# Kernel tuning notes

Hardware: AMD Instinct MI355X
Metric: run time of the kernel (lower is better)

The kernel has to match this reference:

```python
import jax, jax.numpy as jnp
import numpy as np

EMBED = 1024
ADIM = 1024
H = 16
HD = ADIM // H          # 64
RAY = 48                # ray_subdim
R = RAY // 3            # 16
SCALE = 1.0 / np.sqrt(HD)
NB = 768                # boundary tokens
MN = 8                  # max neighbors
FG = 6                  # face_group
L = 1024                # tokens per face
B = 12                  # b * face_group
STAGES = 4


def _apply_dray(x, d, einsum_str, inverse):
    ray = x[..., :RAY].reshape(x.shape[:-1] + (3, R))
    if inverse:
        d = jnp.swapaxes(d, -1, -2)
    ray = jnp.einsum(einsum_str, d, ray).reshape(x.shape[:-1] + (RAY,))
    return jnp.concatenate([ray, x[..., RAY:]], axis=-1)


def setup_inputs() -> dict:
    key = jax.random.key(0)
    ks = jax.random.split(key, 12)
    inp = {}
    inp['x'] = jax.random.normal(ks[0], (B, L, EMBED), dtype=jnp.float32)
    inp['qkv_w'] = jax.random.normal(ks[1], (EMBED, 3 * ADIM), dtype=jnp.float32) * 0.02
    inp['out_w'] = jax.random.normal(ks[2], (ADIM, EMBED), dtype=jnp.float32) * 0.02
    inp['out_b'] = jax.random.normal(ks[3], (EMBED,), dtype=jnp.float32) * 0.02
    inp['d_ray'] = jax.random.normal(ks[4], (STAGES, FG, L, 3, 3), dtype=jnp.float32)
    inp['boundary_face_ids'] = jax.random.randint(ks[5], (NB,), 0, FG, dtype=jnp.int32).astype(jnp.int64)
    inp['boundary_token_indices'] = jnp.arange(NB, dtype=jnp.int64)
    inp['boundary_local_indices'] = jax.random.randint(ks[6], (NB,), 0, L, dtype=jnp.int32).astype(jnp.int64)
    inp['boundary_stage_ids'] = jax.random.randint(ks[7], (NB,), 0, STAGES, dtype=jnp.int32).astype(jnp.int64)
    inp['neighbor_face_ids'] = jax.random.randint(ks[8], (NB, MN), 0, FG, dtype=jnp.int32).astype(jnp.int64)
    inp['neighbor_token_indices'] = jax.random.randint(ks[9], (NB, MN), 0, L, dtype=jnp.int32).astype(jnp.int64)
    inp['neighbor_local_indices'] = jax.random.randint(ks[10], (NB, MN), 0, L, dtype=jnp.int32).astype(jnp.int64)
    inp['neighbor_stage_ids'] = jax.random.randint(ks[11], (NB, MN), 0, STAGES, dtype=jnp.int32).astype(jnp.int64)
    inp['neighbor_mask'] = jnp.ones((NB, MN), dtype=bool)
    inp['face_group'] = FG
    return inp


def reference(x, qkv_w, out_w, out_b, d_ray,
              boundary_face_ids, boundary_token_indices, boundary_local_indices, boundary_stage_ids,
              neighbor_face_ids, neighbor_token_indices, neighbor_local_indices, neighbor_stage_ids,
              neighbor_mask, face_group):
    b = x.shape[0] // face_group
    l = x.shape[1]
    xt = x.reshape(b, face_group, l, EMBED)          # [b, FG, L, E]
    max_face, max_idx = face_group - 1, l - 1

    qf = jnp.clip(boundary_face_ids, 0, max_face)
    qi = jnp.clip(boundary_token_indices, 0, max_idx)
    valid_q = (boundary_face_ids == qf) & (boundary_token_indices == qi)

    nf = jnp.clip(neighbor_face_ids, 0, max_face)
    ni = jnp.clip(neighbor_token_indices, 0, max_idx)
    mask = neighbor_mask & (neighbor_face_ids == nf) & (neighbor_token_indices == ni)

    # gather boundary queries and neighbor keys/values
    x_q = xt[:, qf, qi, :]                            # [b, NB, E]
    x_kv = xt[:, nf, ni, :]                           # [b, NB, MN, E]
    q = (x_q @ qkv_w)[..., :ADIM]
    kv = x_kv @ qkv_w
    k = kv[..., ADIM:2 * ADIM]
    v = kv[..., 2 * ADIM:]

    nb, mn = q.shape[1], k.shape[2]
    q = q.reshape(b, nb, H, HD)
    k = k.reshape(b, nb, mn, H, HD)
    v = v.reshape(b, nb, mn, H, HD)

    d_q = d_ray[boundary_stage_ids, boundary_face_ids, boundary_local_indices]     # [NB, 3, 3]
    d_k = d_ray[neighbor_stage_ids,
                jnp.maximum(neighbor_face_ids, 0),
                jnp.maximum(neighbor_local_indices, 0)]                            # [NB, MN, 3, 3]

    q = _apply_dray(q, d_q, 'nij,bnhjr->bnhir', inverse=False)
    k = _apply_dray(k, d_k, 'nmij,bnmhjr->bnmhir', inverse=False)
    v = _apply_dray(v, d_k, 'nmij,bnmhjr->bnmhir', inverse=False)

    attn = jnp.einsum('bnhd,bnmhd->bnmh', q, k) * SCALE
    attn = jnp.where(mask[None, :, :, None], attn, -jnp.inf)
    attn = jax.nn.softmax(attn, axis=2)               # softmax over neighbors
    out = jnp.einsum('bnmh,bnmhd->bnhd', attn, v)

    out = _apply_dray(out, d_q, 'nij,bnhjr->bnhir', inverse=True)
    out = out.reshape(b, nb, ADIM) @ out_w + out_b
    out = out * valid_q[None, :, None].astype(out.dtype)

    out_full = jnp.zeros_like(xt).at[:, qf, qi, :].set(out)
    return out_full.reshape(-1, l, EMBED)
```

## Files before the change

### kernel.cpp

```cpp
#include <hip/hip_runtime.h>
#include <hip/hip_bf16.h>
#include <cstddef>

#define FG 6
#define L 1024
#define NB 768
#define MN 8
#define H 16
#define HD 64
#define ADIM 1024
#define STAGES 4
#define SCALE 0.125f

typedef __attribute__((ext_vector_type(8))) short bf16x8;
typedef __attribute__((ext_vector_type(4))) float f32x4;
typedef __attribute__((address_space(3))) short lds_short_t;
typedef const __attribute__((address_space(1))) short g_short_t;

__device__ __forceinline__ int clampi(int v, int lo, int hi) {
  return v < lo ? lo : (v > hi ? hi : v);
}

__device__ __forceinline__ short f2bf(float f) {
  __hip_bfloat16 h = __float2bfloat16(f);
  return *reinterpret_cast<short*>(&h);
}

__device__ __forceinline__ float bf2f(short s) {
  __hip_bfloat16 h = *reinterpret_cast<__hip_bfloat16*>(&s);
  return __bfloat162float(h);
}

__device__ __forceinline__ void gload16(const short* g, short* l) {
  __builtin_amdgcn_global_load_lds((g_short_t*)g, (lds_short_t*)l, 16, 0, 0);
}

__global__ __launch_bounds__(256)
void prep_kernel(const float* __restrict__ in, short* __restrict__ out,
                 float* __restrict__ zout) {
  const size_t zi = ((size_t)blockIdx.x * 256 + threadIdx.x) * 4;
  *(float4*)(zout + zi) = (float4){0.f, 0.f, 0.f, 0.f};
  if (blockIdx.x >= 6144) return;
  size_t i = ((size_t)blockIdx.x * 256 + threadIdx.x) * 8;
  float4 a = *(const float4*)(in + i);
  float4 b = *(const float4*)(in + i + 4);
  bf16x8 v;
  v[0] = f2bf(a.x); v[1] = f2bf(a.y); v[2] = f2bf(a.z); v[3] = f2bf(a.w);
  v[4] = f2bf(b.x); v[5] = f2bf(b.y); v[6] = f2bf(b.z); v[7] = f2bf(b.w);
  *(bf16x8*)(out + i) = v;
}

__global__ __launch_bounds__(256)
void transpose_both(const float* __restrict__ qkv_w, short* __restrict__ qwT,
                    const float* __restrict__ out_w, short* __restrict__ owT) {
  const int z = blockIdx.z;
  if (z == 1 && blockIdx.x >= 32) return;
  const float* in = z ? out_w : qkv_w;
  short* out = z ? owT : qwT;
  const int N = z ? 1024 : 3072;
  __shared__ float tile[32][33];
  const int n0 = blockIdx.x * 32, k0 = blockIdx.y * 32;
  const int tx = threadIdx.x & 31, ty = threadIdx.x >> 5;
  #pragma unroll
  for (int i = 0; i < 4; ++i)
    tile[ty + i * 8][tx] = in[(size_t)(k0 + ty + i * 8) * N + n0 + tx];
  __syncthreads();
  #pragma unroll
  for (int i = 0; i < 4; ++i)
    out[(size_t)(n0 + ty + i * 8) * 1024 + k0 + tx] =
        f2bf(tile[tx][ty + i * 8]);
}

__global__ __launch_bounds__(256)
void q_gemm64(const short* __restrict__ A, const short* __restrict__ B,
              float* __restrict__ C,
              const int* __restrict__ f_ids, const int* __restrict__ t_ids)
{
  __shared__ __align__(16) short As[4096];
  __shared__ __align__(16) short Bs[8192];

  const int tid = threadIdx.x;
  const int w = tid >> 6, lane = tid & 63;
  const int row0 = blockIdx.y * 64, col0 = blockIdx.x * 128;
  const int lr = lane & 15, lq = lane >> 4;
  const int wrow = (w >> 1) * 32, wcol = (w & 1) * 64;

  size_t asrc[2]; short* adst[2];
  #pragma unroll
  for (int c = 0; c < 2; ++c) {
    const int d = c * 256 + tid, r = d >> 3;
    const int ss = (d & 7) ^ (r & 7);
    const int rr = row0 + r;
    const int bi = rr >= NB;
    const int idx = rr - bi * NB;
    const int f = clampi(f_ids[idx], 0, FG - 1);
    const int q = clampi(t_ids[idx], 0, L - 1);
    asrc[c] = (size_t)((bi * FG + f) * L + q) * 1024 + ss * 8;
    adst[c] = As + d * 8;
  }
  size_t bsrc[4]; short* bdst[4];
  #pragma unroll
  for (int c = 0; c < 4; ++c) {
    const int d = c * 256 + tid, r = d >> 3;
    const int ss = (d & 7) ^ (r & 7);
    bsrc[c] = (size_t)(col0 + r) * 1024 + ss * 8;
    bdst[c] = Bs + d * 8;
  }

  const char* As8 = (const char*)As;
  const char* Bs8 = (const char*)Bs;
  const int swz = lr & 7;

  f32x4 acc[2][4];
  #pragma unroll
  for (int m = 0; m < 2; ++m)
    #pragma unroll
    for (int n = 0; n < 4; ++n) acc[m][n] = (f32x4){0.f, 0.f, 0.f, 0.f};

  for (int kt = 0; kt < 16; ++kt) {
    #pragma unroll
    for (int c = 0; c < 2; ++c) gload16(A + asrc[c] + kt * 64, adst[c]);
    #pragma unroll
    for (int c = 0; c < 4; ++c) gload16(B + bsrc[c] + kt * 64, bdst[c]);
    __syncthreads();
    #pragma unroll
    for (int kk = 0; kk < 2; ++kk) {
      const int so = ((kk * 4 + lq) ^ swz) << 4;
      bf16x8 av[2], bv[4];
      #pragma unroll
      for (int m = 0; m < 2; ++m)
        av[m] = *(const bf16x8*)(As8 + (wrow + m * 16 + lr) * 128 + so);
      #pragma unroll
      for (int n = 0; n < 4; ++n)
        bv[n] = *(const bf16x8*)(Bs8 + (wcol + n * 16 + lr) * 128 + so);
      #pragma unroll
      for (int m = 0; m < 2; ++m)
        #pragma unroll
        for (int n = 0; n < 4; ++n)
          acc[m][n] = __builtin_amdgcn_mfma_f32_16x16x32_bf16(
              av[m], bv[n], acc[m][n], 0, 0, 0);
    }
    __syncthreads();
  }

  #pragma unroll
  for (int m = 0; m < 2; ++m)
    #pragma unroll
    for (int j = 0; j < 4; ++j) {
      const int r = row0 + wrow + m * 16 + lq * 4 + j;
      #pragma unroll
      for (int n = 0; n < 4; ++n)
        C[(size_t)r * 1024 + col0 + wcol + n * 16 + lr] = acc[m][n][j];
    }
}

#define BAR()   do { __builtin_amdgcn_s_barrier(); __builtin_amdgcn_sched_barrier(0); } while (0)
#define LGKM(N) do { asm volatile("s_waitcnt lgkmcnt(" #N ")" ::: "memory"); __builtin_amdgcn_sched_barrier(0); } while (0)
#define VMC(N)  do { asm volatile("s_waitcnt vmcnt(" #N ")" ::: "memory"); __builtin_amdgcn_sched_barrier(0); } while (0)
#define PRIO1   __builtin_amdgcn_s_setprio(1)
#define PRIO0   __builtin_amdgcn_s_setprio(0)

#define LDA6(D, FB, KK, BUF)                                                  \
  { _Pragma("unroll")                                                         \
    for (int f_ = 0; f_ < 3; ++f_) {                                          \
      const int row_ = (2 * ((FB) + f_) + wm) * 16 + lr;                      \
      D[f_] = *(const bf16x8*)(As8 + (BUF) * 24576 + row_ * 128               \
               + ((((KK) * 4 + lq) ^ swz) << 4));                             \
    } }

#define LDB4(D, KK, BUF)                                                      \
  { _Pragma("unroll")                                                         \
    for (int g_ = 0; g_ < 4; ++g_) {                                          \
      const int row_ = wn * 64 + g_ * 16 + lr;                                \
      D[g_] = *(const bf16x8*)(Bs8 + (BUF) * 32768 + row_ * 128               \
               + ((((KK) * 4 + lq) ^ swz) << 4));                             \
    } }

#define MM6(AV, BV, FB)                                                       \
  { _Pragma("unroll")                                                         \
    for (int f_ = 0; f_ < 3; ++f_)                                            \
      _Pragma("unroll")                                                       \
      for (int g_ = 0; g_ < 4; ++g_)                                          \
        acc[(FB) + f_][g_] = __builtin_amdgcn_mfma_f32_16x16x32_bf16(         \
            AV[f_], BV[g_], acc[(FB) + f_][g_], 0, 0, 0); }

__global__ __launch_bounds__(512, 2)
void kv_gemm192(const short* __restrict__ A, const short* __restrict__ B,
                short* __restrict__ C,
                const int* __restrict__ f_ids, const int* __restrict__ t_ids)
{
  __shared__ __align__(16) short As[24576];
  __shared__ __align__(16) short Bs[32768];

  const int tid = threadIdx.x;
  const int w = tid >> 6, lane = tid & 63;
  const int wm = w >> 2, wn = w & 3;
  const int lr = lane & 15, lq = lane >> 4;
  const int row0 = blockIdx.y * 192;
  const int col0 = blockIdx.x * 256;

  const int ssrc = (((tid & 7) ^ ((tid >> 3) & 7))) * 8;

  size_t a_src[3];
  #pragma unroll
  for (int c = 0; c < 3; ++c) {
    const int rr = row0 + c * 64 + (tid >> 3);
    const int bi = rr >= NB * MN;
    const int idx = rr - bi * (NB * MN);
    const int f = clampi(f_ids[idx], 0, FG - 1);
    const int q = clampi(t_ids[idx], 0, L - 1);
    a_src[c] = (size_t)((bi * FG + f) * L + q) * 1024 + ssrc;
  }
  size_t b_src[2][2];
  #pragma unroll
  for (int h = 0; h < 2; ++h)
    #pragma unroll
    for (int i = 0; i < 2; ++i)
      b_src[h][i] = (size_t)(1024 + col0 + h * 128 + ((tid + i * 512) >> 3)) * 1024 + ssrc;

  auto stgA = [&](int c, int kt, int buf) {
    gload16(A + a_src[c] + kt * 64, As + buf * 12288 + c * 4096 + tid * 8);
  };
  auto stgB = [&](int h, int kt, int buf) {
    gload16(B + b_src[h][0] + kt * 64, Bs + buf * 16384 + h * 8192 + tid * 8);
    gload16(B + b_src[h][1] + kt * 64, Bs + buf * 16384 + h * 8192 + 4096 + tid * 8);
  };

  const char* As8 = (const char*)As;
  const char* Bs8 = (const char*)Bs;
  const int swz = lane & 7;

  f32x4 acc[6][4];
  #pragma unroll
  for (int f = 0; f < 6; ++f)
    #pragma unroll
    for (int g = 0; g < 4; ++g) acc[f][g] = (f32x4){0.f, 0.f, 0.f, 0.f};

  bf16x8 avA[3], avB[3], bv0[4], bv1[4];

  stgB(0, 0, 0); stgB(1, 0, 0); stgA(0, 0, 0); stgA(1, 0, 0); stgA(2, 0, 0);
  stgB(0, 1, 1); stgB(1, 1, 1); stgA(0, 1, 1);
  VMC(5); BAR();

  for (int I = 0; I < 7; ++I) {
    const int kA = 2 * I + 1, kB = 2 * I + 2, kC = 2 * I + 3;
    LDA6(avA, 0, 0, 0); LDB4(bv0, 0, 0); stgA(1, kA, 1);
    BAR(); LGKM(0); PRIO1; MM6(avA, bv0, 0); PRIO0; BAR();
    LDA6(avB, 0, 1, 0); LDB4(bv1, 1, 0); stgA(2, kA, 1);
    BAR(); LGKM(0); PRIO1; MM6(avB, bv1, 0); PRIO0; BAR();
    LDA6(avA, 3, 0, 0); stgB(0, kB, 0);
    BAR(); LGKM(0); PRIO1; MM6(avA, bv0, 3); PRIO0; BAR();
    LDA6(avB, 3, 1, 0); stgB(1, kB, 0); stgA(0, kB, 0);
    BAR(); LGKM(0); PRIO1; MM6(avB, bv1, 3); PRIO0; VMC(5); BAR();
    LDA6(avA, 0, 0, 1); LDB4(bv0, 0, 1); stgA(1, kB, 0);
    BAR(); LGKM(0); PRIO1; MM6(avA, bv0, 0); PRIO0; BAR();
    LDA6(avB, 0, 1, 1); LDB4(bv1, 1, 1); stgA(2, kB, 0);
    BAR(); LGKM(0); PRIO1; MM6(avB, bv1, 0); PRIO0; BAR();
    LDA6(avA, 3, 0, 1); stgB(0, kC, 1);
    BAR(); LGKM(0); PRIO1; MM6(avA, bv0, 3); PRIO0; BAR();
    LDA6(avB, 3, 1, 1); stgB(1, kC, 1); stgA(0, kC, 1);
    BAR(); LGKM(0); PRIO1; MM6(avB, bv1, 3); PRIO0; VMC(5); BAR();
  }

  {
    LDA6(avA, 0, 0, 0); LDB4(bv0, 0, 0); stgA(1, 15, 1);
    BAR(); LGKM(0); PRIO1; MM6(avA, bv0, 0); PRIO0; BAR();

    LDA6(avB, 0, 1, 0); LDB4(bv1, 1, 0); stgA(2, 15, 1);
    BAR(); LGKM(0); PRIO1; MM6(avB, bv1, 0); PRIO0; BAR();

    LDA6(avA, 3, 0, 0);
    BAR(); LGKM(0); PRIO1; MM6(avA, bv0, 3); PRIO0; BAR();

    LDA6(avB, 3, 1, 0);
    BAR(); LGKM(0); PRIO1; MM6(avB, bv1, 3); PRIO0; VMC(0); BAR();

    LDA6(avA, 0, 0, 1); LDB4(bv0, 0, 1);
    BAR(); LGKM(0); PRIO1; MM6(avA, bv0, 0); PRIO0; BAR();

    LDA6(avB, 0, 1, 1); LDB4(bv1, 1, 1);
    BAR(); LGKM(0); PRIO1; MM6(avB, bv1, 0); PRIO0; BAR();

    LDA6(avA, 3, 0, 1);
    BAR(); LGKM(0); PRIO1; MM6(avA, bv0, 3); PRIO0; BAR();

    LDA6(avB, 3, 1, 1);
    BAR(); LGKM(0); PRIO1; MM6(avB, bv1, 3); PRIO0;
  }

  #pragma unroll
  for (int f = 0; f < 6; ++f) {
    #pragma unroll
    for (int j = 0; j < 4; ++j) {
      const int r = row0 + (2 * f + wm) * 16 + lq * 4 + j;
      short* cp = C + (size_t)r * 2048 + col0 + wn * 64 + lr;
      #pragma unroll
      for (int g = 0; g < 4; ++g)
        cp[g * 16] = f2bf(acc[f][g][j]);
    }
  }
}

__global__ __launch_bounds__(256)
void out_gemm64(const short* __restrict__ A, const short* __restrict__ B,
                float* __restrict__ C,
                const int* __restrict__ f_ids, const int* __restrict__ t_ids,
                const float* __restrict__ bias)
{
  __shared__ __align__(16) short As[4096];
  __shared__ __align__(16) short Bs[8192];

  const int tid = threadIdx.x;
  const int w = tid >> 6, lane = tid & 63;
  const int row0 = blockIdx.y * 64, col0 = blockIdx.x * 128;
  const int lr = lane & 15, lq = lane >> 4;
  const int wrow = (w >> 1) * 32, wcol = (w & 1) * 64;

  size_t asrc[2]; short* adst[2];
  #pragma unroll
  for (int c = 0; c < 2; ++c) {
    const int d = c * 256 + tid, r = d >> 3;
    const int ss = (d & 7) ^ (r & 7);
    asrc[c] = (size_t)(row0 + r) * 1024 + ss * 8;
    adst[c] = As + d * 8;
  }
  size_t bsrc[4]; short* bdst[4];
  #pragma unroll
  for (int c = 0; c < 4; ++c) {
    const int d = c * 256 + tid, r = d >> 3;
    const int ss = (d & 7) ^ (r & 7);
    bsrc[c] = (size_t)(col0 + r) * 1024 + ss * 8;
    bdst[c] = Bs + d * 8;
  }

  const char* As8 = (const char*)As;
  const char* Bs8 = (const char*)Bs;
  const int swz = lr & 7;

  f32x4 acc[2][4];
  #pragma unroll
  for (int m = 0; m < 2; ++m)
    #pragma unroll
    for (int n = 0; n < 4; ++n) acc[m][n] = (f32x4){0.f, 0.f, 0.f, 0.f};

  for (int kt = 0; kt < 16; ++kt) {
    #pragma unroll
    for (int c = 0; c < 2; ++c) gload16(A + asrc[c] + kt * 64, adst[c]);
    #pragma unroll
    for (int c = 0; c < 4; ++c) gload16(B + bsrc[c] + kt * 64, bdst[c]);
    __syncthreads();
    #pragma unroll
    for (int kk = 0; kk < 2; ++kk) {
      const int so = ((kk * 4 + lq) ^ swz) << 4;
      bf16x8 av[2], bv[4];
      #pragma unroll
      for (int m = 0; m < 2; ++m)
        av[m] = *(const bf16x8*)(As8 + (wrow + m * 16 + lr) * 128 + so);
      #pragma unroll
      for (int n = 0; n < 4; ++n)
        bv[n] = *(const bf16x8*)(Bs8 + (wcol + n * 16 + lr) * 128 + so);
      #pragma unroll
      for (int m = 0; m < 2; ++m)
        #pragma unroll
        for (int n = 0; n < 4; ++n)
          acc[m][n] = __builtin_amdgcn_mfma_f32_16x16x32_bf16(
              av[m], bv[n], acc[m][n], 0, 0, 0);
    }
    __syncthreads();
  }

  float bb[4];
  #pragma unroll
  for (int n = 0; n < 4; ++n) bb[n] = bias[col0 + wcol + n * 16 + lr];
  #pragma unroll
  for (int m = 0; m < 2; ++m)
    #pragma unroll
    for (int j = 0; j < 4; ++j) {
      const int r  = row0 + wrow + m * 16 + lq * 4 + j;
      const int bi = r >= NB;
      const int nn = r - bi * NB;
      const int bf = f_ids[nn], bt = t_ids[nn];
      const int qf = clampi(bf, 0, FG - 1), qi = clampi(bt, 0, L - 1);
      const bool valid = (bf == qf) && (bt == qi);
      const size_t obase = ((size_t)(bi * FG + qf) * L + qi) * 1024;
      #pragma unroll
      for (int n = 0; n < 4; ++n) {
        const int col = col0 + wcol + n * 16 + lr;
        C[obase + col] = valid ? (acc[m][n][j] + bb[n]) : 0.f;
      }
    }
}

__global__ __launch_bounds__(256)
void attn_kernel2(const float* __restrict__ dray,
                  const int* __restrict__ bfid, const int* __restrict__ blid,
                  const int* __restrict__ bsid,
                  const int* __restrict__ nfid, const int* __restrict__ ntid,
                  const int* __restrict__ nlid, const int* __restrict__ nsid,
                  const int* __restrict__ nmask,
                  const float* __restrict__ qbuf,
                  const short* __restrict__ kvbuf,
                  __hip_bfloat16* __restrict__ obuf)
{
  __shared__ __align__(16) short kvlds[MN * 2048];
  __shared__ float smdq[9];
  __shared__ float smdk[MN][9];
  __shared__ int   smok[MN];

  const int bn   = blockIdx.x;
  const int n    = bn % NB;
  const int tid  = threadIdx.x;
  const int w    = tid >> 6, lane = tid & 63;

  const short* kvb = kvbuf + (size_t)bn * MN * 2048;
  #pragma unroll
  for (int j = 0; j < 8; ++j)
    gload16(kvb + (j * 256 + tid) * 8, kvlds + (j * 256 + tid) * 8);

  if (tid < 9) {
    int st = clampi(bsid[n], 0, STAGES - 1);
    int f  = clampi(bfid[n], 0, FG - 1);
    int lc = clampi(blid[n], 0, L - 1);
    smdq[tid] = dray[((size_t)(st * FG + f) * L + lc) * 9 + tid];
  } else if (tid >= 64 && tid < 136) {
    const int t = tid - 64, m = t / 9, j = t - m * 9;
    const int idx = n * MN + m;
    int nst = clampi(nsid[idx], 0, STAGES - 1);
    int nfc = clampi(nfid[idx], 0, FG - 1);
    int nlc = clampi(nlid[idx], 0, L - 1);
    smdk[m][j] = dray[((size_t)(nst * FG + nfc) * L + nlc) * 9 + j];
  } else if (tid >= 192 && tid < 192 + MN) {
    const int m = tid - 192;
    const int idx = n * MN + m;
    int nf = nfid[idx], nt = ntid[idx];
    smok[m] = (nmask[idx] != 0) && nf >= 0 && nf < FG && nt >= 0 && nt < L;
  }
  __syncthreads();

  float dq[9];
  #pragma unroll
  for (int t = 0; t < 9; ++t) dq[t] = smdq[t];

  const int rr = lane & 15;

  for (int hi = 0; hi < 4; ++hi) {
    const int h = hi * 4 + w;

    const float qraw = qbuf[(size_t)bn * ADIM + h * HD + lane];
    float x0 = __shfl(qraw, rr), x1 = __shfl(qraw, 16 + rr), x2 = __shfl(qraw, 32 + rr);
    float q0 = dq[0]*x0 + dq[1]*x1 + dq[2]*x2;
    float q1 = dq[3]*x0 + dq[4]*x1 + dq[5]*x2;
    float q2 = dq[6]*x0 + dq[7]*x1 + dq[8]*x2;
    float qd = lane < 16 ? q0 : lane < 32 ? q1 : lane < 48 ? q2 : qraw;

    float s[MN], vd[MN];
    #pragma unroll
    for (int m = 0; m < MN; ++m) {
      float dk[9];
      #pragma unroll
      for (int t = 0; t < 9; ++t) dk[t] = smdk[m][t];

      float kraw = bf2f(kvlds[m * 2048 + h * HD + lane]);
      float k0 = __shfl(kraw, rr), k1 = __shfl(kraw, 16 + rr), k2 = __shfl(kraw, 32 + rr);
      float kr0 = dk[0]*k0 + dk[1]*k1 + dk[2]*k2;
      float kr1 = dk[3]*k0 + dk[4]*k1 + dk[5]*k2;
      float kr2 = dk[6]*k0 + dk[7]*k1 + dk[8]*k2;
      float kd = lane < 16 ? kr0 : lane < 32 ? kr1 : lane < 48 ? kr2 : kraw;

      float p = qd * kd;
      #pragma unroll
      for (int off = 32; off; off >>= 1) p += __shfl_xor(p, off);
      s[m] = p;

      float vraw = bf2f(kvlds[m * 2048 + 1024 + h * HD + lane]);
      float v0 = __shfl(vraw, rr), v1 = __shfl(vraw, 16 + rr), v2 = __shfl(vraw, 32 + rr);
      float vr0 = dk[0]*v0 + dk[1]*v1 + dk[2]*v2;
      float vr1 = dk[3]*v0 + dk[4]*v1 + dk[5]*v2;
      float vr2 = dk[6]*v0 + dk[7]*v1 + dk[8]*v2;
      vd[m] = lane < 16 ? vr0 : lane < 32 ? vr1 : lane < 48 ? vr2 : vraw;
    }

    float mx = -INFINITY;
    #pragma unroll
    for (int m = 0; m < MN; ++m) {
      s[m] = smok[m] ? s[m] * SCALE : -INFINITY;
      mx = fmaxf(mx, s[m]);
    }
    float den = 0.f;
    #pragma unroll
    for (int m = 0; m < MN; ++m) { s[m] = expf(s[m] - mx); den += s[m]; }
    float inv = 1.0f / den;

    float od = 0.f;
    #pragma unroll
    for (int m = 0; m < MN; ++m) od += s[m] * vd[m];
    od *= inv;

    float y0 = __shfl(od, rr), y1 = __shfl(od, 16 + rr), y2 = __shfl(od, 32 + rr);
    float t0 = dq[0]*y0 + dq[3]*y1 + dq[6]*y2;
    float t1 = dq[1]*y0 + dq[4]*y1 + dq[7]*y2;
    float t2 = dq[2]*y0 + dq[5]*y1 + dq[8]*y2;
    float outd = lane < 16 ? t0 : lane < 32 ? t1 : lane < 48 ? t2 : od;

    obuf[(size_t)bn * ADIM + h * HD + lane] = __float2bfloat16(outd);
  }
}

extern "C" void kernel_launch(void* const* d_in, const int* in_sizes, int n_in,
                              void* d_out, int out_size, void* d_ws, size_t ws_size,
                              hipStream_t stream) {
  const float* x     = (const float*)d_in[0];
  const float* qkv_w = (const float*)d_in[1];
  const float* out_w = (const float*)d_in[2];
  const float* out_b = (const float*)d_in[3];
  const float* dray  = (const float*)d_in[4];
  const int* bfid  = (const int*)d_in[5];
  const int* btid  = (const int*)d_in[6];
  const int* blid  = (const int*)d_in[7];
  const int* bsid  = (const int*)d_in[8];
  const int* nfid  = (const int*)d_in[9];
  const int* ntid  = (const int*)d_in[10];
  const int* nlid  = (const int*)d_in[11];
  const int* nsid  = (const int*)d_in[12];
  const int* nmask = (const int*)d_in[13];

  char* ws = (char*)d_ws;
  short* xb    = (short*)(ws);
  short* qwT   = (short*)(ws + 25165824);
  short* owT   = (short*)(ws + 31457280);
  float* qbuf  = (float*)(ws + 33554432);
  short* kvbuf = (short*)(ws + 39845888);
  short* obuf  = (short*)(ws + 90177536);

  prep_kernel<<<12288, 256, 0, stream>>>(x, xb, (float*)d_out);
  transpose_both<<<dim3(96, 32, 2), 256, 0, stream>>>(qkv_w, qwT, out_w, owT);

  q_gemm64<<<dim3(8, 24), 256, 0, stream>>>(xb, qwT, qbuf, bfid, btid);
  kv_gemm192<<<dim3(8, 64), 512, 0, stream>>>(xb, qwT, kvbuf, nfid, ntid);
  attn_kernel2<<<1536, 256, 0, stream>>>(dray, bfid, blid, bsid,
                                         nfid, ntid, nlid, nsid, nmask,
                                         qbuf, kvbuf,
                                         (__hip_bfloat16*)obuf);
  out_gemm64<<<dim3(8, 24), 256, 0, stream>>>(obuf, owT, (float*)d_out,
                                              bfid, btid, out_b);
}
```

Measured before the change: 158.7 us.

## Merge prep and transpose kernels; coarsen kv GEMM pipeline into fewer barrier phases

The x conversion/zeroing kernel and the weight-transpose kernel are merged into one launch, with blocks dispatched by block index, which removes one kernel launch and its tail. The kv_gemm192 main loop now issues two LDS fragment loads and two MFMA groups per barrier phase instead of one. This halves the number of barrier pairs per K step. The cost is more live registers and less interleaving between LDS reads and MFMAs.

```diff
diff --git a/kernel.cpp b/kernel.cpp
--- a/kernel.cpp
+++ b/kernel.cpp
@@ -36,30 +36,29 @@
 }
 
 __global__ __launch_bounds__(256)
-void prep_kernel(const float* __restrict__ in, short* __restrict__ out,
-                 float* __restrict__ zout) {
-  const size_t zi = ((size_t)blockIdx.x * 256 + threadIdx.x) * 4;
-  *(float4*)(zout + zi) = (float4){0.f, 0.f, 0.f, 0.f};
-  if (blockIdx.x >= 6144) return;
-  size_t i = ((size_t)blockIdx.x * 256 + threadIdx.x) * 8;
-  float4 a = *(const float4*)(in + i);
-  float4 b = *(const float4*)(in + i + 4);
-  bf16x8 v;
-  v[0] = f2bf(a.x); v[1] = f2bf(a.y); v[2] = f2bf(a.z); v[3] = f2bf(a.w);
-  v[4] = f2bf(b.x); v[5] = f2bf(b.y); v[6] = f2bf(b.z); v[7] = f2bf(b.w);
-  *(bf16x8*)(out + i) = v;
-}
-
-__global__ __launch_bounds__(256)
-void transpose_both(const float* __restrict__ qkv_w, short* __restrict__ qwT,
-                    const float* __restrict__ out_w, short* __restrict__ owT) {
-  const int z = blockIdx.z;
-  if (z == 1 && blockIdx.x >= 32) return;
-  const float* in = z ? out_w : qkv_w;
-  short* out = z ? owT : qwT;
-  const int N = z ? 1024 : 3072;
+void prep_kernel(const float* __restrict__ x, short* __restrict__ xb,
+                 float* __restrict__ zout,
+                 const float* __restrict__ qkv_w, short* __restrict__ qwT,
+                 const float* __restrict__ out_w, short* __restrict__ owT) {
+  const int b = blockIdx.x;
+  if (b < 12288) {
+    const size_t zi = ((size_t)b * 256 + threadIdx.x) * 4;
+    *(float4*)(zout + zi) = (float4){0.f, 0.f, 0.f, 0.f};
+    if (b >= 6144) return;
+    size_t i = ((size_t)b * 256 + threadIdx.x) * 8;
+    float4 a = *(const float4*)(x + i);
+    float4 c = *(const float4*)(x + i + 4);
+    bf16x8 v;
+    v[0] = f2bf(a.x); v[1] = f2bf(a.y); v[2] = f2bf(a.z); v[3] = f2bf(a.w);
+    v[4] = f2bf(c.x); v[5] = f2bf(c.y); v[6] = f2bf(c.z); v[7] = f2bf(c.w);
+    *(bf16x8*)(xb + i) = v;
+    return;
+  }
+  int t = b - 12288;
+  const float* in; short* out; int N, n0, k0;
+  if (t < 3072) { in = qkv_w; out = qwT; N = 3072; n0 = (t % 96) * 32; k0 = (t / 96) * 32; }
+  else { t -= 3072; in = out_w; out = owT; N = 1024; n0 = (t % 32) * 32; k0 = (t / 32) * 32; }
   __shared__ float tile[32][33];
-  const int n0 = blockIdx.x * 32, k0 = blockIdx.y * 32;
   const int tx = threadIdx.x & 31, ty = threadIdx.x >> 5;
   #pragma unroll
   for (int i = 0; i < 4; ++i)
@@ -154,6 +153,7 @@
     }
 }
 
+
 #define BAR()   do { __builtin_amdgcn_s_barrier(); __builtin_amdgcn_sched_barrier(0); } while (0)
 #define LGKM(N) do { asm volatile("s_waitcnt lgkmcnt(" #N ")" ::: "memory"); __builtin_amdgcn_sched_barrier(0); } while (0)
 #define VMC(N)  do { asm volatile("s_waitcnt vmcnt(" #N ")" ::: "memory"); __builtin_amdgcn_sched_barrier(0); } while (0)
@@ -244,48 +244,33 @@
 
   for (int I = 0; I < 7; ++I) {
     const int kA = 2 * I + 1, kB = 2 * I + 2, kC = 2 * I + 3;
-    LDA6(avA, 0, 0, 0); LDB4(bv0, 0, 0); stgA(1, kA, 1);
-    BAR(); LGKM(0); PRIO1; MM6(avA, bv0, 0); PRIO0; BAR();
-    LDA6(avB, 0, 1, 0); LDB4(bv1, 1, 0); stgA(2, kA, 1);
-    BAR(); LGKM(0); PRIO1; MM6(avB, bv1, 0); PRIO0; BAR();
-    LDA6(avA, 3, 0, 0); stgB(0, kB, 0);
-    BAR(); LGKM(0); PRIO1; MM6(avA, bv0, 3); PRIO0; BAR();
-    LDA6(avB, 3, 1, 0); stgB(1, kB, 0); stgA(0, kB, 0);
-    BAR(); LGKM(0); PRIO1; MM6(avB, bv1, 3); PRIO0; VMC(5); BAR();
-    LDA6(avA, 0, 0, 1); LDB4(bv0, 0, 1); stgA(1, kB, 0);
-    BAR(); LGKM(0); PRIO1; MM6(avA, bv0, 0); PRIO0; BAR();
-    LDA6(avB, 0, 1, 1); LDB4(bv1, 1, 1); stgA(2, kB, 0);
-    BAR(); LGKM(0); PRIO1; MM6(avB, bv1, 0); PRIO0; BAR();
-    LDA6(avA, 3, 0, 1); stgB(0, kC, 1);
-    BAR(); LGKM(0); PRIO1; MM6(avA, bv0, 3); PRIO0; BAR();
-    LDA6(avB, 3, 1, 1); stgB(1, kC, 1); stgA(0, kC, 1);
-    BAR(); LGKM(0); PRIO1; MM6(avB, bv1, 3); PRIO0; VMC(5); BAR();
+    LDA6(avA, 0, 0, 0); LDB4(bv0, 0, 0); LDA6(avB, 0, 1, 0); LDB4(bv1, 1, 0);
+    stgA(1, kA, 1); stgA(2, kA, 1);
+    BAR(); LGKM(0); PRIO1; MM6(avA, bv0, 0); MM6(avB, bv1, 0); PRIO0; BAR();
+    LDA6(avA, 3, 0, 0); LDA6(avB, 3, 1, 0);
+    stgB(0, kB, 0); stgB(1, kB, 0); stgA(0, kB, 0);
+    BAR(); LGKM(0); PRIO1; MM6(avA, bv0, 3); MM6(avB, bv1, 3); PRIO0; VMC(5); BAR();
+    LDA6(avA, 0, 0, 1); LDB4(bv0, 0, 1); LDA6(avB, 0, 1, 1); LDB4(bv1, 1, 1);
+    stgA(1, kB, 0); stgA(2, kB, 0);
+    BAR(); LGKM(0); PRIO1; MM6(avA, bv0, 0); MM6(avB, bv1, 0); PRIO0; BAR();
+    LDA6(avA, 3, 0, 1); LDA6(avB, 3, 1, 1);
+    stgB(0, kC, 1); stgB(1, kC, 1); stgA(0, kC, 1);
+    BAR(); LGKM(0); PRIO1; MM6(avA, bv0, 3); MM6(avB, bv1, 3); PRIO0; VMC(5); BAR();
   }
 
   {
-    LDA6(avA, 0, 0, 0); LDB4(bv0, 0, 0); stgA(1, 15, 1);
-    BAR(); LGKM(0); PRIO1; MM6(avA, bv0, 0); PRIO0; BAR();
-
-    LDA6(avB, 0, 1, 0); LDB4(bv1, 1, 0); stgA(2, 15, 1);
-    BAR(); LGKM(0); PRIO1; MM6(avB, bv1, 0); PRIO0; BAR();
-
-    LDA6(avA, 3, 0, 0);
-    BAR(); LGKM(0); PRIO1; MM6(avA, bv0, 3); PRIO0; BAR();
-
-    LDA6(avB, 3, 1, 0);
-    BAR(); LGKM(0); PRIO1; MM6(avB, bv1, 3); PRIO0; VMC(0); BAR();
-
-    LDA6(avA, 0, 0, 1); LDB4(bv0, 0, 1);
-    BAR(); LGKM(0); PRIO1; MM6(avA, bv0, 0); PRIO0; BAR();
-
-    LDA6(avB, 0, 1, 1); LDB4(bv1, 1, 1);
-    BAR(); LGKM(0); PRIO1; MM6(avB, bv1, 0); PRIO0; BAR();
-
-    LDA6(avA, 3, 0, 1);
-    BAR(); LGKM(0); PRIO1; MM6(avA, bv0, 3); PRIO0; BAR();
-
-    LDA6(avB, 3, 1, 1);
-    BAR(); LGKM(0); PRIO1; MM6(avB, bv1, 3); PRIO0;
+    LDA6(avA, 0, 0, 0); LDB4(bv0, 0, 0); LDA6(avB, 0, 1, 0); LDB4(bv1, 1, 0);
+    stgA(1, 15, 1); stgA(2, 15, 1);
+    BAR(); LGKM(0); PRIO1; MM6(avA, bv0, 0); MM6(avB, bv1, 0); PRIO0; BAR();
+
+    LDA6(avA, 3, 0, 0); LDA6(avB, 3, 1, 0);
+    BAR(); LGKM(0); PRIO1; MM6(avA, bv0, 3); MM6(avB, bv1, 3); PRIO0; VMC(0); BAR();
+
+    LDA6(avA, 0, 0, 1); LDB4(bv0, 0, 1); LDA6(avB, 0, 1, 1); LDB4(bv1, 1, 1);
+    BAR(); LGKM(0); PRIO1; MM6(avA, bv0, 0); MM6(avB, bv1, 0); PRIO0; BAR();
+
+    LDA6(avA, 3, 0, 1); LDA6(avB, 3, 1, 1);
+    BAR(); LGKM(0); PRIO1; MM6(avA, bv0, 3); MM6(avB, bv1, 3); PRIO0;
   }
 
   #pragma unroll
@@ -532,8 +517,8 @@
   short* kvbuf = (short*)(ws + 39845888);
   short* obuf  = (short*)(ws + 90177536);
 
-  prep_kernel<<<12288, 256, 0, stream>>>(x, xb, (float*)d_out);
-  transpose_both<<<dim3(96, 32, 2), 256, 0, stream>>>(qkv_w, qwT, out_w, owT);
+  prep_kernel<<<16384, 256, 0, stream>>>(x, xb, (float*)d_out,
+                                         qkv_w, qwT, out_w, owT);
 
   q_gemm64<<<dim3(8, 24), 256, 0, stream>>>(xb, qwT, qbuf, bfid, btid);
   kv_gemm192<<<dim3(8, 64), 512, 0, stream>>>(xb, qwT, kvbuf, nfid, ntid);
```

Measured after the change: 154.8 us. -2.4%, faster.
